# Kernel tuning notes

Hardware: AMD Instinct MI355X
Metric: run time of the kernel (lower is better)

Reference implementation:

```python
import jax, jax.numpy as jnp
import numpy as np

INPUT_DIM = 8192
HIDDEN = 512
EMBED = HIDDEN // 2  # op embedding dim
NUM_TEMPERS = 64
NUM_OPS = 3
MAX_HOPS = 4
B = 2048


def setup_inputs() -> dict:
    key = jax.random.key(0)
    ks = jax.random.split(key, 10)
    n = lambda k, shape: jax.random.normal(k, shape, jnp.float32)
    return {
        "x": n(ks[0], (B, INPUT_DIM)),
        "op_emb": 0.01 * n(ks[1], (NUM_OPS, EMBED)),
        "op_logits": jnp.zeros((NUM_OPS,), jnp.float32),
        "id_embeds": 0.01 * n(ks[2], (128, 4)),
        "W1": n(ks[3], (HIDDEN + 4 + EMBED, HIDDEN)) / np.sqrt(HIDDEN + 4 + EMBED),
        "b1": jnp.zeros((HIDDEN,), jnp.float32),
        "W2": n(ks[4], (HIDDEN, HIDDEN)) / np.sqrt(HIDDEN),
        "b2": jnp.zeros((HIDDEN,), jnp.float32),
        "Wr1": n(ks[5], (HIDDEN + 4, 32)) / np.sqrt(HIDDEN + 4),
        "br1": jnp.zeros((32,), jnp.float32),
        "Wr2": n(ks[6], (32, NUM_TEMPERS + 1)) / np.sqrt(32),
        "br2": jnp.zeros((NUM_TEMPERS + 1,), jnp.float32),
        "Wp": n(ks[7], (HIDDEN, INPUT_DIM)) / np.sqrt(HIDDEN),
        "bp": jnp.zeros((INPUT_DIM,), jnp.float32),
        "tid_emb": 0.01 * n(ks[8], (NUM_TEMPERS, 4)),
        "rng_seed": 42,
    }


def reference(x, op_emb, op_logits, id_embeds, W1, b1, W2, b2, Wr1, br1, Wr2, br2, Wp, bp, tid_emb, rng_seed):
    Bx, D = x.shape
    # D is a multiple of HIDDEN here -> no padding branch needed
    num_patches = D // HIDDEN
    patch_states = x.reshape(Bx * num_patches, HIDDEN)
    N = patch_states.shape[0]

    rng = jax.random.key(rng_seed)
    rng, tk = jax.random.split(rng)
    patch_tempers = jax.random.randint(tk, (N,), 0, NUM_TEMPERS)
    patch_done = jnp.zeros((N,), bool)

    # Fixed-length unroll of the while_loop (max_hops=4). Early-exit only
    # differs if ALL patches stop early, which is vanishingly unlikely.
    for hop in range(MAX_HOPS):
        # --- gather active patches (inactive slots fill with index 0, as in original) ---
        active_idx = jnp.where(~patch_done, size=N, fill_value=0)[0]
        x_active = patch_states[active_idx]          # [N, HIDDEN]
        t_active = patch_tempers[active_idx]         # [N]
        # --- Temper: sample op per patch, embed, 2-layer relu MLP ---
        rng, ok = jax.random.split(rng)
        op_probs = jax.nn.softmax(op_logits)
        op_idx = jax.random.categorical(ok, jnp.log(op_probs), shape=(N,))
        x_aug = jnp.concatenate([x_active, id_embeds[t_active], op_emb[op_idx]], axis=-1)
        h = jax.nn.relu(x_aug @ W1 + b1)
        h = jax.nn.relu(h @ W2 + b2)                 # [N, HIDDEN]
        # --- scatter back updated states ---
        patch_states = patch_states.at[active_idx].set(h)
        # --- routing policy + categorical sampling of next temper / stop ---
        enriched = jnp.concatenate([h, tid_emb[t_active]], axis=-1)
        logits = jax.nn.relu(enriched @ Wr1 + br1) @ Wr2 + br2
        rng, sk = jax.random.split(rng)
        sampled = jax.random.categorical(sk, jax.nn.log_softmax(logits))
        stop = sampled == NUM_TEMPERS
        next_t = jnp.clip(sampled, 0, NUM_TEMPERS - 1)
        patch_tempers = patch_tempers.at[active_idx].set(next_t)
        patch_done = patch_done.at[active_idx].set(stop)

    latent = patch_states.reshape(Bx, num_patches, HIDDEN).mean(axis=1)  # [B, HIDDEN]
    pred = latent @ Wp + bp                                              # [B, INPUT_DIM]
    return latent, pred
```

## Files before the change

kernel.cpp:

```cpp
#include <hip/hip_runtime.h>
#include <cstdint>
#include <cstddef>


#define NPATCH 32768
#define NHOP 4
#define RSCALE 4096.0f
#define RINV   2.44140625e-4f

typedef unsigned short u16;
typedef __attribute__((ext_vector_type(8))) _Float16 half8;
typedef __attribute__((ext_vector_type(4))) float f32x4;

#define GLDS(gp, lp) __builtin_amdgcn_global_load_lds( \
    (const __attribute__((address_space(1))) void*)(const void*)(gp), \
    (__attribute__((address_space(3))) void*)(void*)(lp), 16, 0, 0)

__device__ __forceinline__ uint32_t rotl32(uint32_t x, int r){ return (x<<r)|(x>>(32-r)); }

__device__ __forceinline__ void tf2x32(uint32_t k0, uint32_t k1, uint32_t x0, uint32_t x1,
                                       uint32_t& o0, uint32_t& o1){
  uint32_t k2 = k0 ^ k1 ^ 0x1BD11BDAu;
  x0 += k0; x1 += k1;
#define TFR(r) { x0 += x1; x1 = rotl32(x1,(r)); x1 ^= x0; }
  TFR(13) TFR(15) TFR(26) TFR(6)   x0 += k1; x1 += k2 + 1u;
  TFR(17) TFR(29) TFR(16) TFR(24)  x0 += k2; x1 += k0 + 2u;
  TFR(13) TFR(15) TFR(26) TFR(6)   x0 += k0; x1 += k1 + 3u;
  TFR(17) TFR(29) TFR(16) TFR(24)  x0 += k1; x1 += k2 + 4u;
  TFR(13) TFR(15) TFR(26) TFR(6)   x0 += k2; x1 += k0 + 5u;
#undef TFR
  o0 = x0; o1 = x1;
}

__device__ __forceinline__ uint32_t jbits32(uint32_t k0, uint32_t k1, uint32_t idx){
  uint32_t a, b; tf2x32(k0, k1, 0u, idx, a, b);
  return a ^ b;
}

__device__ __forceinline__ void jsplit(uint32_t& r0, uint32_t& r1, uint32_t& c0, uint32_t& c1){
  uint32_t n0, n1;
  tf2x32(r0, r1, 0u, 0u, n0, n1);
  tf2x32(r0, r1, 0u, 1u, c0, c1);
  r0 = n0; r1 = n1;
}

__device__ __forceinline__ float jgumbel(uint32_t bits){
  float f = __uint_as_float(0x3f800000u | (bits >> 9)) - 1.0f;
  float u = fmaxf(f, 1.17549435e-38f);
  return -logf(-logf(u));
}

union uhcv { _Float16 h; u16 u; };
__device__ __forceinline__ u16 f2h(float x){ uhcv t; t.h = (_Float16)x; return t.u; }
__device__ __forceinline__ float h2f(u16 b){ uhcv t; t.u = b; return (float)t.h; }
__device__ __forceinline__ void split2s(float v, u16& a0, u16& a1){
  a0 = f2h(v);
  a1 = f2h((v - h2f(a0)) * RSCALE);
}

__global__ void k_keys(const int* __restrict__ seed, const float* __restrict__ op_logits,
                       uint32_t* __restrict__ keys, float* __restrict__ logp3){
  if (threadIdx.x != 0 || blockIdx.x != 0) return;
  uint32_t r0 = 0u, r1 = (uint32_t)seed[0];
  uint32_t c0, c1;
  jsplit(r0, r1, c0, c1); keys[0] = c0; keys[1] = c1;
  for (int h = 0; h < NHOP; h++){
    jsplit(r0, r1, c0, c1); keys[2 + 4*h] = c0; keys[3 + 4*h] = c1;
    jsplit(r0, r1, c0, c1); keys[4 + 4*h] = c0; keys[5 + 4*h] = c1;
  }
  float l0 = op_logits[0], l1 = op_logits[1], l2 = op_logits[2];
  float mm = fmaxf(l0, fmaxf(l1, l2));
  float e0 = expf(l0-mm), e1 = expf(l1-mm), e2 = expf(l2-mm);
  float ssum = e0 + e1 + e2;
  logp3[0] = logf(e0/ssum); logp3[1] = logf(e1/ssum); logp3[2] = logf(e2/ssum);
}

__global__ __launch_bounds__(256)
void k_init(const uint32_t* __restrict__ keys, int* __restrict__ tempers, int* __restrict__ done){
  int i = blockIdx.x*256 + threadIdx.x;
  uint32_t b = jbits32(keys[0], keys[1], (uint32_t)(NPATCH + i));
  tempers[i] = (int)(b & 63u);
  done[i] = 0;
}

__global__ __launch_bounds__(256)
void k_precomp(const float* __restrict__ id_embeds, const float* __restrict__ op_emb,
               const float* __restrict__ tid_emb,
               const float* __restrict__ W1, const float* __restrict__ b1,
               const float* __restrict__ Wr1, const float* __restrict__ br1,
               float* __restrict__ idW, float* __restrict__ opWb, float* __restrict__ tidWb){
  int b = blockIdx.x, tid = threadIdx.x;
  if (b < 64){
    for (int j = tid; j < 512; j += 256){
      float v = 0.f;
      #pragma unroll
      for (int u = 0; u < 4; u++) v = fmaf(id_embeds[b*4+u], W1[(size_t)(512+u)*512 + j], v);
      idW[b*512 + j] = v;
    }
  } else if (b < 67){
    int o = b - 64;
    for (int j = tid; j < 512; j += 256){
      float v = b1[j];
      for (int u = 0; u < 256; u++) v = fmaf(op_emb[o*256+u], W1[(size_t)(516+u)*512 + j], v);
      opWb[o*512 + j] = v;
    }
  } else {
    for (int idx = tid; idx < 2048; idx += 256){
      int t = idx >> 5, c = idx & 31;
      float v = br1[c];
      #pragma unroll
      for (int u = 0; u < 4; u++) v = fmaf(tid_emb[t*4+u], Wr1[(512+u)*32 + c], v);
      tidWb[idx] = v;
    }
  }
}

__global__ __launch_bounds__(256)
void k_splitW(const float* __restrict__ W1, const float* __restrict__ W2,
              const float* __restrict__ Wp, const float* __restrict__ Wr1,
              u16* __restrict__ W1T, u16* __restrict__ W2T, u16* __restrict__ WpT,
              u16* __restrict__ Wr1P){
  __shared__ float t[32][33];
  int blk = blockIdx.x;
  const float* src; u16* dst; int N; int deg; size_t pst; int tb;
  if (blk < 256){ src = W1; dst = W1T; N = 512; deg = 2; pst = (size_t)512*512; tb = blk; }
  else if (blk < 512){ src = W2; dst = W2T; N = 512; deg = 2; pst = (size_t)512*512; tb = blk - 256; }
  else if (blk < 528){ src = Wr1; dst = Wr1P; N = 32; deg = 2; pst = (size_t)32*512; tb = blk - 512; }
  else { src = Wp; dst = WpT; N = 8192; deg = 1; pst = 0; tb = blk - 528; }
  int n0 = (tb >> 4)*32, k0 = (tb & 15)*32;
  if (N == 32){ n0 = 0; k0 = tb*32; }
  int r = threadIdx.x >> 5, c = threadIdx.x & 31;
  for (int rr = r; rr < 32; rr += 8)
    t[rr][c] = src[(size_t)(k0+rr)*N + ((n0 + c) % N)];
  __syncthreads();
  for (int rr = r; rr < 32; rr += 8){
    if (n0 + rr >= N) break;
    float v = t[c][rr];
    size_t o = (size_t)(n0+rr)*512 + k0 + c;
    if (deg == 2){
      u16 a0, a1; split2s(v, a0, a1);
      dst[o] = a0; dst[pst + o] = a1;
    } else {
      dst[o] = f2h(v);
    }
  }
}

__global__ __launch_bounds__(256)
void k_xsplit(const float* __restrict__ x, u16* __restrict__ sP){
  size_t i = ((size_t)blockIdx.x*256 + threadIdx.x)*4;
  float4 v = *(const float4*)(x + i);
  ushort4 p0, p1;
  split2s(v.x, p0.x, p1.x); split2s(v.y, p0.y, p1.y);
  split2s(v.z, p0.z, p1.z); split2s(v.w, p0.w, p1.w);
  const size_t SP = (size_t)NPATCH*512;
  *(ushort4*)(sP + i) = p0; *(ushort4*)(sP + SP + i) = p1;
}

__global__ __launch_bounds__(1024)
void k_scan(const int* __restrict__ done, int* __restrict__ aidx, int* __restrict__ meta){
  __shared__ int cnt[1024];
  int tid = threadIdx.x;
  int base = tid * 32;
  unsigned flags = 0; int c = 0;
  #pragma unroll
  for (int i = 0; i < 32; i++){
    int f = (done[base + i] == 0);
    flags |= ((unsigned)f) << i;
    c += f;
  }
  cnt[tid] = c;
  __syncthreads();
  int val = c;
  for (int off = 1; off < 1024; off <<= 1){
    int v = (tid >= off) ? cnt[tid - off] : 0;
    __syncthreads();
    val += v; cnt[tid] = val;
    __syncthreads();
  }
  int pos = val - c;
  for (int i = 0; i < 32; i++){
    if ((flags >> i) & 1u) aidx[pos++] = base + i;
  }
  __syncthreads();
  int na = cnt[1023];
  for (int j = na + tid; j < NPATCH; j += 1024) aidx[j] = 0;
  if (tid == 0){
    meta[0] = na;
    meta[1] = (na < NPATCH) ? (NPATCH - 1) : 0;
  }
}

__global__ __launch_bounds__(256)
void k_gather(const int* __restrict__ aidx, const int* __restrict__ tempers,
              const uint32_t* __restrict__ keys, const float* __restrict__ logp3,
              int hop, int* __restrict__ t_act, int* __restrict__ op_idx){
  int s = blockIdx.x*256 + threadIdx.x;
  int p = aidx[s];
  t_act[s] = tempers[p];
  uint32_t k0 = keys[2 + 4*hop], k1 = keys[3 + 4*hop];
  float best = 0.f; int bi = 0;
  #pragma unroll
  for (int c = 0; c < 3; c++){
    float v = jgumbel(jbits32(k0, k1, (uint32_t)(3*s + c))) + logp3[c];
    if (c == 0 || v > best){ best = v; bi = c; }
  }
  op_idx[s] = bi;
}

template<int MODE, int DEG>
__global__ __launch_bounds__(256, 2)
void k_mgemm(const u16* __restrict__ Ap, const u16* __restrict__ Bp,
             float* __restrict__ outF, u16* __restrict__ outP,
             const int* __restrict__ aidx, const float* __restrict__ bias,
             const float* __restrict__ idW, const float* __restrict__ opWb,
             const int* __restrict__ t_act, const int* __restrict__ op_idx,
             const int* __restrict__ meta,
             int Ncols, size_t aStride, size_t bStride, size_t oStride){
  __shared__ u16 As[2*DEG*4096];
  __shared__ u16 Bs[2*DEG*4096];
  const int tid = threadIdx.x;
  const int L = tid & 63, w = tid >> 6;

  const int gx = (int)gridDim.x;
  const int nwg = gx * (int)gridDim.y;
  int lin = (int)blockIdx.y * gx + (int)blockIdx.x;
  if ((nwg & 7) == 0)
    lin = (lin & 7) * (nwg >> 3) + (lin >> 3);
  const int m0 = (lin / gx) * 128, n0 = (lin % gx) * 128;
  const int wr = w >> 1, wc = w & 1;

  constexpr int SPW = DEG*4;
  constexpr int BUFO = DEG*4096;
  const bool isA = (w < 2);
  const u16* gB = isA ? Ap : Bp;
  u16* lB = isA ? As : Bs;
  const size_t pstride = isA ? aStride : bStride;
  const u16* gseg[8];
  u16* lseg[8];
  #pragma unroll
  for (int q = 0; q < SPW; q++){
    int ss = (w & 1)*SPW + q;
    int p = ss >> 3, rb = ss & 7;
    int row16 = rb*16 + (L >> 2);
    int grow;
    if (isA) grow = (MODE == 1) ? aidx[m0 + row16] : (m0 + row16);
    else     grow = n0 + row16;
    int swz = (L & 3) ^ ((L >> 2) & 3);
    gseg[q] = gB + p*pstride + (size_t)grow*512 + swz*8;
    lseg[q] = lB + p*4096 + rb*512;
  }

  f32x4 accM[4][4], accR[4][4];
  #pragma unroll
  for (int i = 0; i < 4; i++)
    #pragma unroll
    for (int j = 0; j < 4; j++){ accM[i][j] = (f32x4)0.f; accR[i][j] = (f32x4)0.f; }

  const int rdsw = ((L >> 4) ^ (L & 3))*8;
  const int frow = L & 15;

  #pragma unroll
  for (int q = 0; q < SPW; q++)
    GLDS(gseg[q], lseg[q]);

  #pragma unroll 2
  for (int kt = 0; kt < 16; kt++){
    const int cb = (kt & 1) * BUFO;
    if (kt < 15){
      const int nb = ((kt + 1) & 1) * BUFO;
      #pragma unroll
      for (int q = 0; q < SPW; q++)
        GLDS(gseg[q] + (kt+1)*32, lseg[q] + nb);
      asm volatile("s_waitcnt vmcnt(%0)" :: "n"(SPW) : "memory");
    } else {
      asm volatile("s_waitcnt vmcnt(0)" ::: "memory");
    }
    __builtin_amdgcn_s_barrier();
    asm volatile("" ::: "memory");

    __builtin_amdgcn_s_setprio(1);
    #pragma unroll
    for (int pa = 0; pa < DEG; pa++){
      half8 af[4];
      #pragma unroll
      for (int i = 0; i < 4; i++)
        af[i] = *(const half8*)&As[cb + pa*4096 + (wr*64 + i*16 + frow)*32 + rdsw];
      #pragma unroll
      for (int pb = 0; pb < DEG - pa; pb++){
        #pragma unroll
        for (int j = 0; j < 4; j++){
          half8 bf = *(const half8*)&Bs[cb + pb*4096 + (wc*64 + j*16 + frow)*32 + rdsw];
          #pragma unroll
          for (int i = 0; i < 4; i++){
            if (pa + pb == 0)
              accM[i][j] = __builtin_amdgcn_mfma_f32_16x16x32_f16(af[i], bf, accM[i][j], 0, 0, 0);
            else
              accR[i][j] = __builtin_amdgcn_mfma_f32_16x16x32_f16(af[i], bf, accR[i][j], 0, 0, 0);
          }
        }
      }
    }
    __builtin_amdgcn_s_setprio(0);

    asm volatile("" ::: "memory");
    __builtin_amdgcn_s_barrier();
  }

  const int rbase = m0 + wr*64 + (L >> 4)*4;
  const int cbase = n0 + wc*64 + (L & 15);
  const int w0v = (MODE == 3) ? meta[1] : 0;
  #pragma unroll
  for (int i = 0; i < 4; i++){
    #pragma unroll
    for (int reg = 0; reg < 4; reg++){
      int r = rbase + i*16 + reg;
      if (MODE == 1){
        int t = t_act[r], o = op_idx[r];
        #pragma unroll
        for (int j = 0; j < 4; j++){
          int c = cbase + j*16;
          float v = accM[i][j][reg] + RINV*accR[i][j][reg] + idW[t*512 + c] + opWb[o*512 + c];
          v = fmaxf(v, 0.f);
          u16 a0, a1; split2s(v, a0, a1);
          size_t off = (size_t)r*512 + c;
          outP[off] = a0; outP[oStride + off] = a1;
        }
      } else if (MODE == 3){
        int p = aidx[r];
        bool allowed = (p != 0) || (r == w0v);
        #pragma unroll
        for (int j = 0; j < 4; j++){
          int c = cbase + j*16;
          float v = accM[i][j][reg] + RINV*accR[i][j][reg] + bias[c];
          v = fmaxf(v, 0.f);
          if (allowed){
            u16 a0, a1; split2s(v, a0, a1);
            size_t off = (size_t)p*512 + c;
            outP[off] = a0; outP[oStride + off] = a1;
          }
        }
      } else {
        #pragma unroll
        for (int j = 0; j < 4; j++){
          int c = cbase + j*16;
          float v = accM[i][j][reg] + bias[c];
          if (DEG == 2) v += RINV*accR[i][j][reg];
          outF[(size_t)r*Ncols + c] = v;
        }
      }
    }
  }
}

__global__ __launch_bounds__(256, 2)
void k_routemm(const u16* __restrict__ sP, const u16* __restrict__ Wr1P,
               const int* __restrict__ aidx, const int* __restrict__ t_act,
               const float* __restrict__ tidWb, float* __restrict__ l32g){
  __shared__ u16 As[2*2*2048];
  __shared__ u16 Bs[2*2048];
  const int tid = threadIdx.x;
  const int L = tid & 63, w = tid >> 6;
  const int m0 = blockIdx.x*64;
  const size_t SPh = (size_t)NPATCH*512;

  const u16* gseg[2]; u16* lseg[2];
  #pragma unroll
  for (int q = 0; q < 2; q++){
    int ss = w*2 + q;
    int p = ss >> 2, rb = ss & 3;
    int row16 = rb*16 + (L >> 2);
    int grow = aidx[m0 + row16];
    int swz = (L & 3) ^ ((L >> 2) & 3);
    gseg[q] = sP + p*SPh + (size_t)grow*512 + swz*8;
    lseg[q] = As + p*2048 + rb*512;
  }
  const u16* gBp = Wr1P + (size_t)(tid>>7)*16384
                        + (size_t)(((tid>>6)&1)*16 + (tid&15))*512 + ((tid>>4)&3)*8;
  u16* lBp = Bs + w*512;

  f32x4 accM[2], accR[2];
  accM[0] = (f32x4)0.f; accM[1] = (f32x4)0.f;
  accR[0] = (f32x4)0.f; accR[1] = (f32x4)0.f;

  const int rdsw = ((L >> 4) ^ (L & 3))*8;

  #pragma unroll
  for (int q = 0; q < 2; q++) GLDS(gseg[q], lseg[q]);
  GLDS(gBp, lBp);

  #pragma unroll 2
  for (int kt = 0; kt < 16; kt++){
    const int cb  = (kt & 1) * 4096;
    const int cbB = (kt & 1) * 2048;
    if (kt < 15){
      const int nb  = ((kt + 1) & 1) * 4096;
      const int nbB = ((kt + 1) & 1) * 2048;
      #pragma unroll
      for (int q = 0; q < 2; q++)
        GLDS(gseg[q] + (kt+1)*32, lseg[q] + nb);
      GLDS(gBp + (kt+1)*32, lBp + nbB);
      asm volatile("s_waitcnt vmcnt(3)" ::: "memory");
    } else {
      asm volatile("s_waitcnt vmcnt(0)" ::: "memory");
    }
    __builtin_amdgcn_s_barrier();
    asm volatile("" ::: "memory");

    #pragma unroll
    for (int pa = 0; pa < 2; pa++){
      half8 af = *(const half8*)&As[cb + pa*2048 + (w*16 + (L & 15))*32 + rdsw];
      #pragma unroll
      for (int pb = 0; pb < 2 - pa; pb++){
        #pragma unroll
        for (int ct = 0; ct < 2; ct++){
          half8 bf = *(const half8*)&Bs[cbB + (pb*2 + ct)*512 + (L >> 4)*128 + (L & 15)*8];
          if (pa + pb == 0)
            accM[ct] = __builtin_amdgcn_mfma_f32_16x16x32_f16(af, bf, accM[ct], 0, 0, 0);
          else
            accR[ct] = __builtin_amdgcn_mfma_f32_16x16x32_f16(af, bf, accR[ct], 0, 0, 0);
        }
      }
    }

    asm volatile("" ::: "memory");
    __builtin_amdgcn_s_barrier();
  }

  #pragma unroll
  for (int reg = 0; reg < 4; reg++){
    int s = m0 + w*16 + (L >> 4)*4 + reg;
    int t = t_act[s];
    #pragma unroll
    for (int ct = 0; ct < 2; ct++){
      int c = ct*16 + (L & 15);
      float v = accM[ct][reg] + RINV*accR[ct][reg] + tidWb[t*32 + c];
      l32g[(size_t)s*32 + c] = fmaxf(v, 0.f);
    }
  }
}

__global__ __launch_bounds__(256)
void k_sample(const float* __restrict__ l32g, const float* __restrict__ Wr2,
              const float* __restrict__ br2,
              const int* __restrict__ aidx, const int* __restrict__ meta,
              const uint32_t* __restrict__ keys, int hop,
              int* __restrict__ tempers, int* __restrict__ done){
  __shared__ float l32s[8][32];
  const int tid = threadIdx.x;
  const int s0 = blockIdx.x * 8;
  l32s[tid >> 5][tid & 31] = l32g[(size_t)s0*32 + tid];
  __syncthreads();

  const int lane = tid & 63, w = tid >> 6;
  const int half = lane >> 5;
  const uint32_t sk0 = keys[4 + 4*hop], sk1 = keys[5 + 4*hop];
  int smp[2];
  for (int pass = 0; pass < 2; pass++){
    const int psl = w*2 + pass;
    const int ps  = s0 + psl;
    const int c = lane;
    float lg = br2[c];
    #pragma unroll
    for (int k = 0; k < 32; k++) lg = fmaf(l32s[psl][k], Wr2[k*65 + c], lg);
    float lg64 = br2[64];
    #pragma unroll
    for (int k = 0; k < 32; k++) lg64 = fmaf(l32s[psl][k], Wr2[k*65 + 64], lg64);
    float m = lg;
    for (int off = 32; off; off >>= 1) m = fmaxf(m, __shfl_xor(m, off));
    m = fmaxf(m, lg64);
    float se = expf(lg - m);
    for (int off = 32; off; off >>= 1) se += __shfl_xor(se, off);
    se += expf(lg64 - m);
    float Lse = logf(se);
    float g = jgumbel(jbits32(sk0, sk1, (uint32_t)(65*ps + c)));
    float v = (lg - m) - Lse + g;
    int idx = c;
    for (int off = 32; off; off >>= 1){
      float ov = __shfl_xor(v, off);
      int   oi = __shfl_xor(idx, off);
      if (ov > v || (ov == v && oi < idx)){ v = ov; idx = oi; }
    }
    float g64 = jgumbel(jbits32(sk0, sk1, (uint32_t)(65*ps + 64)));
    float v64 = (lg64 - m) - Lse + g64;
    if (v64 > v) idx = 64;
    smp[pass] = idx;
  }

  const int s = s0 + w*2 + half;
  const int mysmp = smp[half];
  const int p = aidx[s];
  const bool allowed = (p != 0) || (s == meta[1]);
  if (allowed && (lane & 31) == 0){
    tempers[p] = (mysmp < 63) ? mysmp : 63;
    done[p]    = (mysmp == 64) ? 1 : 0;
  }
}

__global__ __launch_bounds__(256)
void k_latent2(const u16* __restrict__ sP, float* __restrict__ outF, u16* __restrict__ latP){
  int idx = blockIdx.x*256 + threadIdx.x;
  int b = idx >> 9, j = idx & 511;
  const size_t SP = (size_t)NPATCH*512;
  float s = 0.f;
  #pragma unroll 4
  for (int u = 0; u < 16; u++){
    size_t e = (size_t)(b*16 + u)*512 + j;
    s += h2f(sP[e]) + RINV*h2f(sP[SP + e]);
  }
  s *= 0.0625f;
  outF[idx] = s;
  latP[idx] = f2h(s);
}

template<int MODE>
__global__ __launch_bounds__(256)
void k_gemmF(const float* __restrict__ A, const float* __restrict__ B, float* __restrict__ C,
             int Ncols,
             const int* __restrict__ aidx,
             const float* __restrict__ bias,
             const float* __restrict__ idW, const float* __restrict__ opWb,
             const int* __restrict__ t_act, const int* __restrict__ op_idx){
  __shared__ float As[16][128];
  __shared__ float Bs[16][128];
  const int tid = threadIdx.x;
  const int bx = blockIdx.x, by = blockIdx.y;
  const int tx = tid & 15, ty = tid >> 4;
  const int lr = tid >> 1, lhalf = tid & 1;
  const int srow = by*128 + lr;
  const int arow = (MODE == 1) ? aidx[srow] : srow;
  const float* Ap = A + (size_t)arow*512 + lhalf*8;
  const float* Bp = B + (size_t)(tid >> 4)*Ncols + bx*128 + (tid & 15)*8;

  float acc[8][8];
  #pragma unroll
  for (int i = 0; i < 8; i++)
    #pragma unroll
    for (int j = 0; j < 8; j++) acc[i][j] = 0.f;

  for (int kt = 0; kt < 512; kt += 16){
    float4 a0 = *(const float4*)(Ap + kt);
    float4 a1 = *(const float4*)(Ap + kt + 4);
    float4 g0 = *(const float4*)(Bp + (size_t)kt*Ncols);
    float4 g1 = *(const float4*)(Bp + (size_t)kt*Ncols + 4);
    __syncthreads();
    As[lhalf*8+0][lr] = a0.x; As[lhalf*8+1][lr] = a0.y;
    As[lhalf*8+2][lr] = a0.z; As[lhalf*8+3][lr] = a0.w;
    As[lhalf*8+4][lr] = a1.x; As[lhalf*8+5][lr] = a1.y;
    As[lhalf*8+6][lr] = a1.z; As[lhalf*8+7][lr] = a1.w;
    *(float4*)&Bs[tid>>4][(tid&15)*8]     = g0;
    *(float4*)&Bs[tid>>4][(tid&15)*8 + 4] = g1;
    __syncthreads();
    #pragma unroll
    for (int k = 0; k < 16; k++){
      float4 av0 = *(float4*)&As[k][ty*8];
      float4 av1 = *(float4*)&As[k][ty*8+4];
      float4 bv0 = *(float4*)&Bs[k][tx*4];
      float4 bv1 = *(float4*)&Bs[k][64 + tx*4];
      float av[8] = {av0.x,av0.y,av0.z,av0.w,av1.x,av1.y,av1.z,av1.w};
      float bv[8] = {bv0.x,bv0.y,bv0.z,bv0.w,bv1.x,bv1.y,bv1.z,bv1.w};
      #pragma unroll
      for (int i = 0; i < 8; i++)
        #pragma unroll
        for (int j = 0; j < 8; j++)
          acc[i][j] = fmaf(av[i], bv[j], acc[i][j]);
    }
  }

  const int col0a = bx*128 + tx*4;
  const int col0b = col0a + 64;
  #pragma unroll
  for (int i = 0; i < 8; i++){
    int s = by*128 + ty*8 + i;
    float adda[4], addb[4];
    if (MODE == 1){
      int t = t_act[s], o = op_idx[s];
      float4 ia = *(const float4*)&idW[t*512 + col0a];
      float4 ib = *(const float4*)&idW[t*512 + col0b];
      float4 oa = *(const float4*)&opWb[o*512 + col0a];
      float4 ob = *(const float4*)&opWb[o*512 + col0b];
      adda[0]=ia.x+oa.x; adda[1]=ia.y+oa.y; adda[2]=ia.z+oa.z; adda[3]=ia.w+oa.w;
      addb[0]=ib.x+ob.x; addb[1]=ib.y+ob.y; addb[2]=ib.z+ob.z; addb[3]=ib.w+ob.w;
    } else {
      float4 ba = *(const float4*)&bias[col0a];
      float4 bb = *(const float4*)&bias[col0b];
      adda[0]=ba.x; adda[1]=ba.y; adda[2]=ba.z; adda[3]=ba.w;
      addb[0]=bb.x; addb[1]=bb.y; addb[2]=bb.z; addb[3]=bb.w;
    }
    float4 va, vb;
    float* pa = &va.x; float* pb = &vb.x;
    #pragma unroll
    for (int j = 0; j < 4; j++){
      float v0 = acc[i][j]   + adda[j];
      float v1 = acc[i][j+4] + addb[j];
      if (MODE != 2){ v0 = fmaxf(v0, 0.f); v1 = fmaxf(v1, 0.f); }
      pa[j] = v0; pb[j] = v1;
    }
    *(float4*)(C + (size_t)s*Ncols + col0a) = va;
    *(float4*)(C + (size_t)s*Ncols + col0b) = vb;
  }
}

__global__ __launch_bounds__(256)
void k_routeF(const float* __restrict__ h2, const float* __restrict__ Wr1,
              const float* __restrict__ Wr2, const float* __restrict__ br2,
              const float* __restrict__ tidWb,
              const int* __restrict__ t_act, const int* __restrict__ aidx,
              const int* __restrict__ meta, const uint32_t* __restrict__ keys, int hop,
              float* __restrict__ states, int* __restrict__ tempers, int* __restrict__ done){
  __shared__ float Wr1s[256][32];
  __shared__ float h2s[8][512];
  __shared__ float l32[8][32];

  const int tid = threadIdx.x;
  const int s0 = blockIdx.x * 8;

  for (int i4 = tid; i4 < 8*128; i4 += 256){
    int sl = i4 >> 7, q = i4 & 127;
    *(float4*)&h2s[sl][q*4] = *(const float4*)&h2[(size_t)(s0+sl)*512 + q*4];
  }

  const int lane = tid & 63, w = tid >> 6;
  const int half = lane >> 5, col = lane & 31;
  const int sl = w*2 + half;
  const int s  = s0 + sl;
  const int t  = t_act[s];
  float acc = tidWb[t*32 + col];

  for (int kh = 0; kh < 2; kh++){
    __syncthreads();
    for (int idx = tid; idx < 256*32; idx += 256)
      Wr1s[idx >> 5][idx & 31] = Wr1[kh*8192 + idx];
    __syncthreads();
    const int kb = kh * 256;
    #pragma unroll 4
    for (int k4 = 0; k4 < 64; k4++){
      float4 hv = *(float4*)&h2s[sl][kb + k4*4];
      acc = fmaf(hv.x, Wr1s[k4*4+0][col], acc);
      acc = fmaf(hv.y, Wr1s[k4*4+1][col], acc);
      acc = fmaf(hv.z, Wr1s[k4*4+2][col], acc);
      acc = fmaf(hv.w, Wr1s[k4*4+3][col], acc);
    }
  }
  l32[sl][col] = fmaxf(acc, 0.f);
  __syncthreads();

  const uint32_t sk0 = keys[4 + 4*hop], sk1 = keys[5 + 4*hop];
  int smp[2];
  for (int pass = 0; pass < 2; pass++){
    const int psl = w*2 + pass;
    const int ps  = s0 + psl;
    const int c = lane;
    float lg = br2[c];
    #pragma unroll
    for (int k = 0; k < 32; k++) lg = fmaf(l32[psl][k], Wr2[k*65 + c], lg);
    float lg64 = br2[64];
    #pragma unroll
    for (int k = 0; k < 32; k++) lg64 = fmaf(l32[psl][k], Wr2[k*65 + 64], lg64);
    float m = lg;
    for (int off = 32; off; off >>= 1) m = fmaxf(m, __shfl_xor(m, off));
    m = fmaxf(m, lg64);
    float se = expf(lg - m);
    for (int off = 32; off; off >>= 1) se += __shfl_xor(se, off);
    se += expf(lg64 - m);
    float Lse = logf(se);
    float g = jgumbel(jbits32(sk0, sk1, (uint32_t)(65*ps + c)));
    float v = (lg - m) - Lse + g;
    int idx = c;
    for (int off = 32; off; off >>= 1){
      float ov = __shfl_xor(v, off);
      int   oi = __shfl_xor(idx, off);
      if (ov > v || (ov == v && oi < idx)){ v = ov; idx = oi; }
    }
    float g64 = jgumbel(jbits32(sk0, sk1, (uint32_t)(65*ps + 64)));
    float v64 = (lg64 - m) - Lse + g64;
    if (v64 > v) idx = 64;
    smp[pass] = idx;
  }

  const int mysmp = smp[half];
  const int p = aidx[s];
  const int w0v = meta[1];
  const bool allowed = (p != 0) || (s == w0v);
  if (allowed){
    const float4* src = (const float4*)&h2s[sl][0];
    float4* dst = (float4*)(states + (size_t)p*512);
    for (int q = col; q < 128; q += 32) dst[q] = src[q];
    if (col == 0){
      tempers[p] = (mysmp < 63) ? mysmp : 63;
      done[p]    = (mysmp == 64) ? 1 : 0;
    }
  }
}

__global__ __launch_bounds__(256)
void k_latentF(const float* __restrict__ states, float* __restrict__ out){
  int idx = blockIdx.x*256 + threadIdx.x;
  int b = idx >> 9, j = idx & 511;
  float s = 0.f;
  #pragma unroll
  for (int u = 0; u < 16; u++) s += states[(size_t)(b*16 + u)*512 + j];
  out[idx] = s * 0.0625f;
}

extern "C" void kernel_launch(void* const* d_in, const int* in_sizes, int n_in,
                              void* d_out, int out_size, void* d_ws, size_t ws_size,
                              hipStream_t stream) {
  (void)in_sizes; (void)n_in; (void)out_size;
  const float* x         = (const float*)d_in[0];
  const float* op_emb    = (const float*)d_in[1];
  const float* op_logits = (const float*)d_in[2];
  const float* id_embeds = (const float*)d_in[3];
  const float* W1        = (const float*)d_in[4];
  const float* b1        = (const float*)d_in[5];
  const float* W2        = (const float*)d_in[6];
  const float* b2        = (const float*)d_in[7];
  const float* Wr1       = (const float*)d_in[8];
  const float* br1       = (const float*)d_in[9];
  const float* Wr2       = (const float*)d_in[10];
  const float* br2       = (const float*)d_in[11];
  const float* Wp        = (const float*)d_in[12];
  const float* bp        = (const float*)d_in[13];
  const float* tid_emb   = (const float*)d_in[14];
  const int*   seed      = (const int*)d_in[15];
  float* out = (float*)d_out;

  char* w = (char*)d_ws;
  uint32_t* keys = (uint32_t*)w;
  float* logp3   = (float*)(w + 256);
  int*   meta    = (int*)(w + 512);
  int*   tempers = (int*)(w + 4096);
  int*   done    = tempers + NPATCH;
  int*   t_act   = done + NPATCH;
  int*   op_idx  = t_act + NPATCH;
  int*   aidx    = op_idx + NPATCH;
  float* idW     = (float*)(aidx + NPATCH);
  float* opWb    = idW + 64*512;
  float* tidWb   = opWb + 3*512;

  const size_t SPh = (size_t)NPATCH*512;
  u16* W1T     = (u16*)(w + (1u<<20));
  u16* W2T     = W1T + (size_t)2*512*512;
  u16* Wr1P    = W2T + (size_t)2*512*512;
  u16* WpT     = Wr1P + (size_t)2*32*512;
  u16* latP    = WpT + (size_t)8192*512;
  u16* statesP = latP + (size_t)2048*512;
  u16* h1P     = statesP + 2*SPh;
  float* l32g  = (float*)(h1P + 2*SPh);
  const size_t NEED = (size_t)((char*)(l32g + (size_t)NPATCH*32) - w);

  k_keys<<<1, 64, 0, stream>>>(seed, op_logits, keys, logp3);
  k_init<<<NPATCH/256, 256, 0, stream>>>(keys, tempers, done);
  k_precomp<<<68, 256, 0, stream>>>(id_embeds, op_emb, tid_emb, W1, b1, Wr1, br1,
                                    idW, opWb, tidWb);

  if (ws_size >= NEED){
    k_splitW<<<4624, 256, 0, stream>>>(W1, W2, Wp, Wr1, W1T, W2T, WpT, Wr1P);
    k_xsplit<<<(NPATCH*512/4)/256, 256, 0, stream>>>(x, statesP);

    for (int hop = 0; hop < NHOP; hop++){
      k_scan<<<1, 1024, 0, stream>>>(done, aidx, meta);
      k_gather<<<NPATCH/256, 256, 0, stream>>>(aidx, tempers, keys, logp3, hop, t_act, op_idx);
      k_mgemm<1,2><<<dim3(4, NPATCH/128), 256, 0, stream>>>(
          statesP, W1T, nullptr, h1P, aidx, nullptr, idW, opWb, t_act, op_idx, meta,
          512, SPh, (size_t)512*512, SPh);
      k_mgemm<3,2><<<dim3(4, NPATCH/128), 256, 0, stream>>>(
          h1P, W2T, nullptr, statesP, aidx, b2, nullptr, nullptr, nullptr, nullptr, meta,
          512, SPh, (size_t)512*512, SPh);
      k_routemm<<<NPATCH/64, 256, 0, stream>>>(statesP, Wr1P, aidx, t_act, tidWb, l32g);
      k_sample<<<NPATCH/8, 256, 0, stream>>>(l32g, Wr2, br2, aidx, meta, keys, hop,
                                             tempers, done);
    }

    k_latent2<<<(2048*512)/256, 256, 0, stream>>>(statesP, out, latP);
    k_mgemm<2,1><<<dim3(64, 16), 256, 0, stream>>>(
        latP, WpT, out + 2048*512, nullptr, nullptr, bp, nullptr, nullptr, nullptr, nullptr,
        nullptr, 8192, (size_t)2048*512, (size_t)8192*512, 0);
  } else {
    const size_t BIG0 = 2u<<20;
    const size_t SB   = (size_t)NPATCH * 512 * sizeof(float);
    float *states, *h1, *h2;
    bool copy_states;
    if (ws_size >= BIG0 + 3*SB){
      states = (float*)(w + BIG0);
      h1     = (float*)(w + BIG0 + SB);
      h2     = (float*)(w + BIG0 + 2*SB);
      copy_states = true;
    } else {
      states = (float*)d_in[0];
      h1     = (float*)(w + BIG0);
      h2     = (float*)(w + BIG0 + SB);
      copy_states = false;
    }
    if (copy_states)
      hipMemcpyAsync(states, x, SB, hipMemcpyDeviceToDevice, stream);

    for (int hop = 0; hop < NHOP; hop++){
      k_scan<<<1, 1024, 0, stream>>>(done, aidx, meta);
      k_gather<<<NPATCH/256, 256, 0, stream>>>(aidx, tempers, keys, logp3, hop, t_act, op_idx);
      k_gemmF<1><<<dim3(4, NPATCH/128), 256, 0, stream>>>(states, W1, h1, 512,
                                      aidx, nullptr, idW, opWb, t_act, op_idx);
      k_gemmF<0><<<dim3(4, NPATCH/128), 256, 0, stream>>>(h1, W2, h2, 512,
                                      nullptr, b2, nullptr, nullptr, nullptr, nullptr);
      k_routeF<<<NPATCH/8, 256, 0, stream>>>(h2, Wr1, Wr2, br2, tidWb, t_act, aidx,
                                      meta, keys, hop, states, tempers, done);
    }

    k_latentF<<<(2048*512)/256, 256, 0, stream>>>(states, out);
    k_gemmF<2><<<dim3(8192/128, 2048/128), 256, 0, stream>>>(out, Wp, out + 2048*512, 8192,
                                      nullptr, bp, nullptr, nullptr, nullptr, nullptr);
  }
}
```

Before: 994.1 us.

## Parallelize active-patch scan, simplify route GEMM, stage Wr2 in LDS

Replaces the single-block compaction scan with a three-kernel multi-block scan (local prefix, partial prefix, scatter) that also folds in the gather of tempers and op sampling. Rewrites the routing GEMM to load fragments straight from global memory into registers, dropping the LDS double buffering and barriers. The sampling kernel now stages Wr2 in shared memory. The scan change adds extra launches and workspace, and the route GEMM gives up coalesced LDS staging.

```diff
diff --git a/kernel.cpp b/kernel.cpp
--- a/kernel.cpp
+++ b/kernel.cpp
@@ -155,6 +155,69 @@
   split2s(v.z, p0.z, p1.z); split2s(v.w, p0.w, p1.w);
   const size_t SP = (size_t)NPATCH*512;
   *(ushort4*)(sP + i) = p0; *(ushort4*)(sP + SP + i) = p1;
+}
+
+__global__ __launch_bounds__(1024)
+void k_scan1(const int* __restrict__ done, int* __restrict__ lpref,
+             int* __restrict__ partials){
+  __shared__ int cnt[1024];
+  const int tid = threadIdx.x;
+  const int e = blockIdx.x*1024 + tid;
+  int f = (done[e] == 0);
+  cnt[tid] = f;
+  __syncthreads();
+  int val = f;
+  for (int off = 1; off < 1024; off <<= 1){
+    int v = (tid >= off) ? cnt[tid - off] : 0;
+    __syncthreads();
+    val += v; cnt[tid] = val;
+    __syncthreads();
+  }
+  lpref[e] = val - f;
+  if (tid == 1023) partials[blockIdx.x] = val;
+}
+
+__global__ void k_scan2(int* __restrict__ partials, int* __restrict__ meta){
+  const int tid = threadIdx.x;
+  int f = (tid < 32) ? partials[tid] : 0;
+  int v = f;
+  #pragma unroll
+  for (int off = 1; off < 32; off <<= 1){
+    int u = __shfl_up(v, off);
+    if (tid >= off) v += u;
+  }
+  if (tid < 32) partials[tid] = v - f;
+  if (tid == 31){
+    meta[0] = v;
+    meta[1] = (v < NPATCH) ? (NPATCH - 1) : 0;
+  }
+}
+
+__global__ __launch_bounds__(1024)
+void k_scan3(const int* __restrict__ done, const int* __restrict__ lpref,
+             const int* __restrict__ partials, const int* __restrict__ meta,
+             const int* __restrict__ tempers,
+             const uint32_t* __restrict__ keys, const float* __restrict__ logp3,
+             int hop, int* __restrict__ aidx, int* __restrict__ t_act,
+             int* __restrict__ op_idx){
+  const int tid = threadIdx.x;
+  const int e = blockIdx.x*1024 + tid;
+  const int base = partials[blockIdx.x];
+  const int lp = lpref[e];
+  const int f = (done[e] == 0);
+  const int na = meta[0];
+  const int pos = f ? (base + lp) : (na + (e - base - lp));
+  const int p = f ? e : 0;
+  aidx[pos] = p;
+  t_act[pos] = tempers[p];
+  const uint32_t k0 = keys[2 + 4*hop], k1 = keys[3 + 4*hop];
+  float best = 0.f; int bi = 0;
+  #pragma unroll
+  for (int c = 0; c < 3; c++){
+    float v = jgumbel(jbits32(k0, k1, (uint32_t)(3*pos + c))) + logp3[c];
+    if (c == 0 || v > best){ best = v; bi = c; }
+  }
+  op_idx[pos] = bi;
 }
 
 __global__ __launch_bounds__(1024)
@@ -353,83 +416,46 @@
   }
 }
 
-__global__ __launch_bounds__(256, 2)
+__global__ __launch_bounds__(256)
 void k_routemm(const u16* __restrict__ sP, const u16* __restrict__ Wr1P,
                const int* __restrict__ aidx, const int* __restrict__ t_act,
                const float* __restrict__ tidWb, float* __restrict__ l32g){
-  __shared__ u16 As[2*2*2048];
-  __shared__ u16 Bs[2*2048];
   const int tid = threadIdx.x;
   const int L = tid & 63, w = tid >> 6;
-  const int m0 = blockIdx.x*64;
+  const int s0 = blockIdx.x*64 + w*16;
   const size_t SPh = (size_t)NPATCH*512;
 
-  const u16* gseg[2]; u16* lseg[2];
-  #pragma unroll
-  for (int q = 0; q < 2; q++){
-    int ss = w*2 + q;
-    int p = ss >> 2, rb = ss & 3;
-    int row16 = rb*16 + (L >> 2);
-    int grow = aidx[m0 + row16];
-    int swz = (L & 3) ^ ((L >> 2) & 3);
-    gseg[q] = sP + p*SPh + (size_t)grow*512 + swz*8;
-    lseg[q] = As + p*2048 + rb*512;
-  }
-  const u16* gBp = Wr1P + (size_t)(tid>>7)*16384
-                        + (size_t)(((tid>>6)&1)*16 + (tid&15))*512 + ((tid>>4)&3)*8;
-  u16* lBp = Bs + w*512;
+  const int arow = aidx[s0 + (L & 15)];
+  const u16* a0p = sP + (size_t)arow*512 + (L >> 4)*8;
+  const u16* a1p = a0p + SPh;
+  const u16* bb = Wr1P + (size_t)(L & 15)*512 + (L >> 4)*8;
+  const size_t BPL = (size_t)32*512;
+  const size_t BCT = (size_t)16*512;
 
   f32x4 accM[2], accR[2];
   accM[0] = (f32x4)0.f; accM[1] = (f32x4)0.f;
   accR[0] = (f32x4)0.f; accR[1] = (f32x4)0.f;
 
-  const int rdsw = ((L >> 4) ^ (L & 3))*8;
-
-  #pragma unroll
-  for (int q = 0; q < 2; q++) GLDS(gseg[q], lseg[q]);
-  GLDS(gBp, lBp);
-
-  #pragma unroll 2
+  #pragma unroll 4
   for (int kt = 0; kt < 16; kt++){
-    const int cb  = (kt & 1) * 4096;
-    const int cbB = (kt & 1) * 2048;
-    if (kt < 15){
-      const int nb  = ((kt + 1) & 1) * 4096;
-      const int nbB = ((kt + 1) & 1) * 2048;
-      #pragma unroll
-      for (int q = 0; q < 2; q++)
-        GLDS(gseg[q] + (kt+1)*32, lseg[q] + nb);
-      GLDS(gBp + (kt+1)*32, lBp + nbB);
-      asm volatile("s_waitcnt vmcnt(3)" ::: "memory");
-    } else {
-      asm volatile("s_waitcnt vmcnt(0)" ::: "memory");
-    }
-    __builtin_amdgcn_s_barrier();
-    asm volatile("" ::: "memory");
-
-    #pragma unroll
-    for (int pa = 0; pa < 2; pa++){
-      half8 af = *(const half8*)&As[cb + pa*2048 + (w*16 + (L & 15))*32 + rdsw];
-      #pragma unroll
-      for (int pb = 0; pb < 2 - pa; pb++){
-        #pragma unroll
-        for (int ct = 0; ct < 2; ct++){
-          half8 bf = *(const half8*)&Bs[cbB + (pb*2 + ct)*512 + (L >> 4)*128 + (L & 15)*8];
-          if (pa + pb == 0)
-            accM[ct] = __builtin_amdgcn_mfma_f32_16x16x32_f16(af, bf, accM[ct], 0, 0, 0);
-          else
-            accR[ct] = __builtin_amdgcn_mfma_f32_16x16x32_f16(af, bf, accR[ct], 0, 0, 0);
-        }
-      }
-    }
-
-    asm volatile("" ::: "memory");
-    __builtin_amdgcn_s_barrier();
+    const int ko = kt*32;
+    half8 a0  = *(const half8*)(a0p + ko);
+    half8 a1  = *(const half8*)(a1p + ko);
+    half8 b00 = *(const half8*)(bb + ko);
+    half8 b01 = *(const half8*)(bb + BCT + ko);
+    half8 b10 = *(const half8*)(bb + BPL + ko);
+    half8 b11 = *(const half8*)(bb + BPL + BCT + ko);
+    accM[0] = __builtin_amdgcn_mfma_f32_16x16x32_f16(a0, b00, accM[0], 0, 0, 0);
+    accM[1] = __builtin_amdgcn_mfma_f32_16x16x32_f16(a0, b01, accM[1], 0, 0, 0);
+    accR[0] = __builtin_amdgcn_mfma_f32_16x16x32_f16(a0, b10, accR[0], 0, 0, 0);
+    accR[1] = __builtin_amdgcn_mfma_f32_16x16x32_f16(a0, b11, accR[1], 0, 0, 0);
+    accR[0] = __builtin_amdgcn_mfma_f32_16x16x32_f16(a1, b00, accR[0], 0, 0, 0);
+    accR[1] = __builtin_amdgcn_mfma_f32_16x16x32_f16(a1, b01, accR[1], 0, 0, 0);
   }
 
   #pragma unroll
   for (int reg = 0; reg < 4; reg++){
-    int s = m0 + w*16 + (L >> 4)*4 + reg;
+    int s = s0 + (L >> 4)*4 + reg;
     int t = t_act[s];
     #pragma unroll
     for (int ct = 0; ct < 2; ct++){
@@ -447,9 +473,11 @@
               const uint32_t* __restrict__ keys, int hop,
               int* __restrict__ tempers, int* __restrict__ done){
   __shared__ float l32s[8][32];
+  __shared__ float Wr2s[32*65];
   const int tid = threadIdx.x;
   const int s0 = blockIdx.x * 8;
   l32s[tid >> 5][tid & 31] = l32g[(size_t)s0*32 + tid];
+  for (int i = tid; i < 32*65; i += 256) Wr2s[i] = Wr2[i];
   __syncthreads();
 
   const int lane = tid & 63, w = tid >> 6;
@@ -462,10 +490,10 @@
     const int c = lane;
     float lg = br2[c];
     #pragma unroll
-    for (int k = 0; k < 32; k++) lg = fmaf(l32s[psl][k], Wr2[k*65 + c], lg);
+    for (int k = 0; k < 32; k++) lg = fmaf(l32s[psl][k], Wr2s[k*65 + c], lg);
     float lg64 = br2[64];
     #pragma unroll
-    for (int k = 0; k < 32; k++) lg64 = fmaf(l32s[psl][k], Wr2[k*65 + 64], lg64);
+    for (int k = 0; k < 32; k++) lg64 = fmaf(l32s[psl][k], Wr2s[k*65 + 64], lg64);
     float m = lg;
     for (int off = 32; off; off >>= 1) m = fmaxf(m, __shfl_xor(m, off));
     m = fmaxf(m, lg64);
@@ -734,9 +762,11 @@
   int*   t_act   = done + NPATCH;
   int*   op_idx  = t_act + NPATCH;
   int*   aidx    = op_idx + NPATCH;
-  float* idW     = (float*)(aidx + NPATCH);
+  int*   lpref   = aidx + NPATCH;
+  float* idW     = (float*)(lpref + NPATCH);
   float* opWb    = idW + 64*512;
   float* tidWb   = opWb + 3*512;
+  int*   partials= (int*)(tidWb + 2048);
 
   const size_t SPh = (size_t)NPATCH*512;
   u16* W1T     = (u16*)(w + (1u<<20));
@@ -759,8 +789,11 @@
     k_xsplit<<<(NPATCH*512/4)/256, 256, 0, stream>>>(x, statesP);
 
     for (int hop = 0; hop < NHOP; hop++){
-      k_scan<<<1, 1024, 0, stream>>>(done, aidx, meta);
-      k_gather<<<NPATCH/256, 256, 0, stream>>>(aidx, tempers, keys, logp3, hop, t_act, op_idx);
+      k_scan1<<<NPATCH/1024, 1024, 0, stream>>>(done, lpref, partials);
+      k_scan2<<<1, 64, 0, stream>>>(partials, meta);
+      k_scan3<<<NPATCH/1024, 1024, 0, stream>>>(done, lpref, partials, meta,
+                                                tempers, keys, logp3, hop,
+                                                aidx, t_act, op_idx);
       k_mgemm<1,2><<<dim3(4, NPATCH/128), 256, 0, stream>>>(
           statesP, W1T, nullptr, h1P, aidx, nullptr, idW, opWb, t_act, op_idx, meta,
           512, SPh, (size_t)512*512, SPh);
```

After: 985.7 us. About the same (-0.8%).
